# Optimization experiments

Measured on AMD Instinct MI355X. Metric: run time of the kernel, lower is better.

## Reference

```python
import jax, jax.numpy as jnp
import numpy as np

B, N, K = 1024, 200, 32
HID = 36
IN_DIM = K * (K + 2)  # k + q + flattened outer product


def setup_inputs() -> dict:
    key = jax.random.key(0)
    ks = jax.random.split(key, 4)
    candidate_ad = jax.random.normal(ks[0], (B, K), dtype=jnp.float32)
    goods = jax.random.normal(ks[1], (B, N, K), dtype=jnp.float32)
    W1 = jax.random.normal(ks[2], (IN_DIM, HID), dtype=jnp.float32) * (1.0 / np.sqrt(IN_DIM))
    b1 = jnp.zeros((HID,), dtype=jnp.float32)
    W2 = jax.random.normal(ks[3], (HID, 1), dtype=jnp.float32) * (1.0 / np.sqrt(HID))
    b2 = jnp.zeros((1,), dtype=jnp.float32)
    return {"candidate_ad": candidate_ad, "goods": goods, "W1": W1, "b1": b1, "W2": W2, "b2": b2}


def reference(candidate_ad, goods, W1, b1, W2, b2):
    # candidate_ad: [B, K] (attention key k), goods: [B, N, K] (queries q per item)
    Bs, Ns, Ks = goods.shape
    # outer product per item: einsum('bi,bj->bij', k, q) vectorized over N -> [B, N, K, K]
    outer = jnp.einsum('bi,bnj->bnij', candidate_ad, goods).reshape(Bs, Ns, Ks * Ks)
    k_b = jnp.broadcast_to(candidate_ad[:, None, :], (Bs, Ns, Ks))
    h1 = jnp.concatenate((k_b, goods, outer), axis=-1)          # [B, N, K*(K+2)]
    act = jax.nn.sigmoid(h1 @ W1 + b1)                           # [B, N, HID]
    weight = act @ W2 + b2                                       # [B, N, 1]
    out = jnp.sum(goods * weight, axis=1)                        # [B, K]
    return out
```

## Files before the change

### kernel.cpp

```cpp
#include <hip/hip_runtime.h>


#define BB 1024
#define BPB 4
#define NN 200
#define KK 32
#define HID 36
#define QP 40
#define LOG2E 1.44269504f

#define QBYTES (BPB * NN * KK * 4)
#define VOFF   QBYTES
#define COFF   (VOFF + 15360)
#define WOFF   (COFF + 768)
#define ROFF   (WOFF + 192)
#define SMEM_TOTAL (ROFF + 2048)

typedef __attribute__((ext_vector_type(8))) short bf16x8;
typedef __attribute__((ext_vector_type(4))) float f32x4;

__device__ __forceinline__ float rfl(float x) {
    return __uint_as_float(__builtin_amdgcn_readfirstlane(__float_as_uint(x)));
}
__device__ __forceinline__ unsigned short f2bf(float x) {
    unsigned int u = __float_as_uint(x);
    u = (u + 0x7fffu + ((u >> 16) & 1u)) >> 16;
    return (unsigned short)u;
}
__device__ __forceinline__ unsigned int pk_bf16(float lo, float hi) {
    unsigned int r;
    asm("v_cvt_pk_bf16_f32 %0, %1, %2" : "=v"(r) : "v"(lo), "v"(hi));
    return r;
}
__device__ __forceinline__ float fast_rcp(float x) {
#if __has_builtin(__builtin_amdgcn_rcpf)
    return __builtin_amdgcn_rcpf(x);
#else
    return 1.0f / x;
#endif
}
__device__ __forceinline__ float fast_exp2(float x) {
#if __has_builtin(__builtin_amdgcn_exp2f)
    return __builtin_amdgcn_exp2f(x);
#else
    return exp2f(x);
#endif
}

__global__ __launch_bounds__(1024, 4) void din_kernel(
    const float* __restrict__ cad,
    const float* __restrict__ goods,
    const float* __restrict__ W1,
    const float* __restrict__ b1p,
    const float* __restrict__ W2,
    const float* __restrict__ b2p,
    float* __restrict__ out)
{
    extern __shared__ char smem[];
    char*           Qlds = smem;
    unsigned short* V16  = (unsigned short*)(smem + VOFF);
    float*          c48  = (float*)(smem + COFF);
    float*          w248 = (float*)(smem + WOFF);
    float*          red_s = (float*)(smem + ROFF);

    const int tid  = threadIdx.x;
    const int b0   = blockIdx.x * BPB;
    const int lane = tid & 63;
    const int wv   = tid >> 6;
    const int l15  = lane & 15, lk = lane >> 4;
    const int bsel = wv & 3;
    const int mrow = wv >> 2;

    if (wv >= 6) {
        const char* gsrc = (const char*)(goods + (size_t)b0 * NN * KK);
        const int loff = (lane * 16) ^ ((lane >> 3) << 4);
        const int ubase = (wv - 6) * 10;
        #pragma unroll
        for (int j = 0; j < 10; ++j) {
            const int u = ubase + j;
            __builtin_amdgcn_global_load_lds(
                (const __attribute__((address_space(1))) void*)(gsrc + u * 1024 + loff),
                (__attribute__((address_space(3))) void*)(Qlds + u * 1024),
                16, 0, 0);
        }
    }

    const float* k0p = cad + b0 * KK;
    const float* k1p = k0p + KK;
    const float* k2p = k1p + KK;
    const float* k3p = k2p + KK;
    const float b2v = rfl(b2p[0]);

    const float4* W1q = reinterpret_cast<const float4*>(W1);
    if (tid < 288) {
        float4 acc0 = W1q[288 + tid];
        float4 acc1 = acc0, acc2 = acc0, acc3 = acc0;
        #pragma unroll 4
        for (int i = 0; i < KK; ++i) {
            const float4 w0 = W1q[576 + 288 * i + tid];
            const float ki0 = k0p[i], ki1 = k1p[i], ki2 = k2p[i], ki3 = k3p[i];
            acc0.x += ki0 * w0.x; acc0.y += ki0 * w0.y;
            acc0.z += ki0 * w0.z; acc0.w += ki0 * w0.w;
            acc1.x += ki1 * w0.x; acc1.y += ki1 * w0.y;
            acc1.z += ki1 * w0.z; acc1.w += ki1 * w0.w;
            acc2.x += ki2 * w0.x; acc2.y += ki2 * w0.y;
            acc2.z += ki2 * w0.z; acc2.w += ki2 * w0.w;
            acc3.x += ki3 * w0.x; acc3.y += ki3 * w0.y;
            acc3.z += ki3 * w0.z; acc3.w += ki3 * w0.w;
        }
        const float a0[4] = {acc0.x, acc0.y, acc0.z, acc0.w};
        const float a1[4] = {acc1.x, acc1.y, acc1.z, acc1.w};
        const float a2[4] = {acc2.x, acc2.y, acc2.z, acc2.w};
        const float a3[4] = {acc3.x, acc3.y, acc3.z, acc3.w};
        #pragma unroll
        for (int q = 0; q < 4; ++q) {
            const int e = 4 * tid + q, j = e / 36, h = e - 36 * j;
            const int o = h * QP + j;
            V16[0 * 1920 + o] = f2bf(a0[q]);
            V16[1 * 1920 + o] = f2bf(a1[q]);
            V16[2 * 1920 + o] = f2bf(a2[q]);
            V16[3 * 1920 + o] = f2bf(a3[q]);
        }
    } else if (tid < 324) {
        const int u = tid - 288, bl = u / 9, hq = u % 9;
        const float* kp = cad + (b0 + bl) * KK;
        float4 acc = reinterpret_cast<const float4*>(b1p)[hq];
        #pragma unroll 4
        for (int i = 0; i < KK; ++i) {
            const float ki = kp[i];
            const float4 wc = W1q[i * 9 + hq];
            acc.x += ki * wc.x; acc.y += ki * wc.y;
            acc.z += ki * wc.z; acc.w += ki * wc.w;
        }
        float4 cp4;
        cp4.x = -acc.x * LOG2E; cp4.y = -acc.y * LOG2E;
        cp4.z = -acc.z * LOG2E; cp4.w = -acc.w * LOG2E;
        *reinterpret_cast<float4*>(&c48[bl * 48 + 4 * hq]) = cp4;
    } else if (tid < 336) {
        const int u = tid - 324, bl = u / 3, q = u % 3;
        *reinterpret_cast<float4*>(&c48[bl * 48 + 36 + 4 * q]) =
            make_float4(0.f, 0.f, 0.f, 0.f);
    } else if (tid < 348) {
        const int u = tid - 336;
        if (u < 9)
            *reinterpret_cast<float4*>(&w248[4 * u]) =
                reinterpret_cast<const float4*>(W2)[u];
        else
            *reinterpret_cast<float4*>(&w248[36 + 4 * (u - 9)]) =
                make_float4(0.f, 0.f, 0.f, 0.f);
    } else if (tid < 732) {
        const int p = tid - 348;
        const int word = p % 192, pair = p / 192;
        const int w = (36 + (word >> 4)) * (QP / 2) + (word & 15);
        ((unsigned int*)V16)[(2 * pair + 0) * 960 + w] = 0u;
        ((unsigned int*)V16)[(2 * pair + 1) * 960 + w] = 0u;
    }
    __syncthreads();

    bf16x8 bfr[3];
    #pragma unroll
    for (int nt = 0; nt < 3; ++nt)
        bfr[nt] = *reinterpret_cast<const bf16x8*>(
            V16 + bsel * 1920 + (nt * 16 + l15) * QP + lk * 8);
    const float* cb = c48 + bsel * 48;

    float facc[8] = {0.f, 0.f, 0.f, 0.f, 0.f, 0.f, 0.f, 0.f};

    auto tile = [&](const float4& qa, const float4& qb, int m, bool masked) {
        union { unsigned int u[4]; bf16x8 v; } aq;
        aq.u[0] = pk_bf16(qa.x, qa.y);
        aq.u[1] = pk_bf16(qa.z, qa.w);
        aq.u[2] = pk_bf16(qb.x, qb.y);
        aq.u[3] = pk_bf16(qb.z, qb.w);
        const f32x4 zero = {0.f, 0.f, 0.f, 0.f};
        const f32x4 d0 = __builtin_amdgcn_mfma_f32_16x16x32_bf16(bfr[0], aq.v, zero, 0, 0, 0);
        const f32x4 d1 = __builtin_amdgcn_mfma_f32_16x16x32_bf16(bfr[1], aq.v, zero, 0, 0, 0);
        const f32x4 d2 = __builtin_amdgcn_mfma_f32_16x16x32_bf16(bfr[2], aq.v, zero, 0, 0, 0);

        const f32x4 c0 = *reinterpret_cast<const f32x4*>(cb + lk * 4);
        const f32x4 w0 = *reinterpret_cast<const f32x4*>(&w248[lk * 4]);
        const f32x4 c1 = *reinterpret_cast<const f32x4*>(cb + 16 + lk * 4);
        const f32x4 w1 = *reinterpret_cast<const f32x4*>(&w248[16 + lk * 4]);
        const f32x4 c2 = *reinterpret_cast<const f32x4*>(cb + 32 + lk * 4);
        const f32x4 w2 = *reinterpret_cast<const f32x4*>(&w248[32 + lk * 4]);

        float p = 0.f;
        #pragma unroll
        for (int r = 0; r < 4; ++r) {
            p += fast_rcp(1.0f + fast_exp2(__builtin_fmaf(d0[r], -LOG2E, c0[r]))) * w0[r];
            p += fast_rcp(1.0f + fast_exp2(__builtin_fmaf(d1[r], -LOG2E, c1[r]))) * w1[r];
            p += fast_rcp(1.0f + fast_exp2(__builtin_fmaf(d2[r], -LOG2E, c2[r]))) * w2[r];
        }
        p += __shfl_xor(p, 16, 64);
        p += __shfl_xor(p, 32, 64);

        float wn = b2v + p;
        if (masked) {
            const int n = m * 16 + l15;
            wn = (n < NN) ? wn : 0.f;
        }
        facc[0] += qa.x * wn; facc[1] += qa.y * wn;
        facc[2] += qa.z * wn; facc[3] += qa.w * wn;
        facc[4] += qb.x * wn; facc[5] += qb.y * wn;
        facc[6] += qb.z * wn; facc[7] += qb.w * wn;
    };

    #pragma unroll
    for (int t = 0; t < 4; ++t) {
        const int m = mrow + 4 * t;
        if (m < 13) {
            int row = m * 16 + l15;
            row = (row < NN) ? row : (NN - 1);
            const int rlin  = bsel * NN + row;
            const int byte0 = rlin * 128 + lk * 32;
            const int swz   = (rlin & 7) << 4;
            const float4 qa = *reinterpret_cast<const float4*>(Qlds + (byte0 ^ swz));
            const float4 qb = *reinterpret_cast<const float4*>(Qlds + ((byte0 + 16) ^ swz));
            tile(qa, qb, m, m == 12);
        }
    }

    #pragma unroll
    for (int s = 1; s <= 8; s <<= 1) {
        #pragma unroll
        for (int u = 0; u < 8; ++u)
            facc[u] += __shfl_xor(facc[u], s, 64);
    }
    if (l15 == 0) {
        #pragma unroll
        for (int u = 0; u < 8; ++u)
            red_s[(bsel * 4 + mrow) * KK + lk * 8 + u] = facc[u];
    }
    __syncthreads();

    if (tid < BPB * KK) {
        const int bl = tid >> 5, j = tid & 31;
        float s = 0.f;
        #pragma unroll
        for (int g = 0; g < 4; ++g) s += red_s[(bl * 4 + g) * KK + j];
        out[(b0 + bl) * KK + j] = s;
    }
}

extern "C" void kernel_launch(void* const* d_in, const int* in_sizes, int n_in,
                              void* d_out, int out_size, void* d_ws, size_t ws_size,
                              hipStream_t stream) {
    const float* cad   = (const float*)d_in[0];
    const float* goods = (const float*)d_in[1];
    const float* W1    = (const float*)d_in[2];
    const float* b1    = (const float*)d_in[3];
    const float* W2    = (const float*)d_in[4];
    const float* b2    = (const float*)d_in[5];
    float* outp = (float*)d_out;

    static bool attr_set = false;
    if (!attr_set) {
        (void)hipFuncSetAttribute((const void*)din_kernel,
                                  hipFuncAttributeMaxDynamicSharedMemorySize,
                                  SMEM_TOTAL);
        attr_set = true;
    }

    din_kernel<<<BB / BPB, 1024, SMEM_TOTAL, stream>>>(cad, goods, W1, b1, W2, b2, outp);
}
```

Before: 15.30 us.

## Split goods LDS prefetch into two phases and overlap second with compute

Reorders the asynchronous global-to-LDS loads of the goods tile so the first 128 rows per batch element arrive before the first barrier. That barrier now waits only with vmcnt(4) instead of a full drain. The first two row tiles are computed while the remaining loads are still in flight, and a second barrier after vmcnt(0) guards the rest. Load work is also redistributed across the loader waves. The aim is to hide part of the global load latency behind the MFMA and sigmoid work. The cost is an extra barrier and reliance on hand-written waitcnt assembly being correct.

Measured after the change: 16.34 us. +6.8%, slower.

```diff
diff --git a/kernel.cpp b/kernel.cpp
--- a/kernel.cpp
+++ b/kernel.cpp
@@ -71,17 +71,34 @@
     const int bsel = wv & 3;
     const int mrow = wv >> 2;
 
+    const float b2v = rfl(b2p[0]);
+    asm volatile("" :: "s"(b2v));
+
     if (wv >= 6) {
         const char* gsrc = (const char*)(goods + (size_t)b0 * NN * KK);
         const int loff = (lane * 16) ^ ((lane >> 3) << 4);
-        const int ubase = (wv - 6) * 10;
-        #pragma unroll
-        for (int j = 0; j < 10; ++j) {
-            const int u = ubase + j;
-            __builtin_amdgcn_global_load_lds(
-                (const __attribute__((address_space(1))) void*)(gsrc + u * 1024 + loff),
-                (__attribute__((address_space(3))) void*)(Qlds + u * 1024),
-                16, 0, 0);
+        const int si = wv - 6;
+        if (si < 8) {
+            #pragma unroll
+            for (int j = 0; j < 8; ++j) {
+                const int g = si * 8 + j;
+                const int u = (g >> 4) * 25 + (g & 15);
+                __builtin_amdgcn_global_load_lds(
+                    (const __attribute__((address_space(1))) void*)(gsrc + u * 1024 + loff),
+                    (__attribute__((address_space(3))) void*)(Qlds + u * 1024),
+                    16, 0, 0);
+            }
+        }
+        if (si < 9) {
+            #pragma unroll
+            for (int j = 0; j < 4; ++j) {
+                const int g = si * 4 + j;
+                const int u = (g / 9) * 25 + 16 + (g % 9);
+                __builtin_amdgcn_global_load_lds(
+                    (const __attribute__((address_space(1))) void*)(gsrc + u * 1024 + loff),
+                    (__attribute__((address_space(3))) void*)(Qlds + u * 1024),
+                    16, 0, 0);
+            }
         }
     }
 
@@ -89,7 +106,6 @@
     const float* k1p = k0p + KK;
     const float* k2p = k1p + KK;
     const float* k3p = k2p + KK;
-    const float b2v = rfl(b2p[0]);
 
     const float4* W1q = reinterpret_cast<const float4*>(W1);
     if (tid < 288) {
@@ -155,7 +171,12 @@
         ((unsigned int*)V16)[(2 * pair + 0) * 960 + w] = 0u;
         ((unsigned int*)V16)[(2 * pair + 1) * 960 + w] = 0u;
     }
-    __syncthreads();
+
+    asm volatile("" ::: "memory");
+    asm volatile("s_waitcnt vmcnt(4) lgkmcnt(0)" ::: "memory");
+    __builtin_amdgcn_sched_barrier(0);
+    __builtin_amdgcn_s_barrier();
+    __builtin_amdgcn_sched_barrier(0);
 
     bf16x8 bfr[3];
     #pragma unroll
@@ -205,17 +226,36 @@
         facc[6] += qb.z * wn; facc[7] += qb.w * wn;
     };
 
+    auto ldq = [&](int m, float4& qa, float4& qb) {
+        int row = m * 16 + l15;
+        row = (row < NN) ? row : (NN - 1);
+        const int rlin  = bsel * NN + row;
+        const int byte0 = rlin * 128 + lk * 32;
+        const int swz   = (rlin & 7) << 4;
+        qa = *reinterpret_cast<const float4*>(Qlds + (byte0 ^ swz));
+        qb = *reinterpret_cast<const float4*>(Qlds + ((byte0 + 16) ^ swz));
+    };
+
     #pragma unroll
-    for (int t = 0; t < 4; ++t) {
+    for (int t = 0; t < 2; ++t) {
+        const int m = mrow + 4 * t;
+        float4 qa, qb;
+        ldq(m, qa, qb);
+        tile(qa, qb, m, false);
+    }
+
+    asm volatile("" ::: "memory");
+    asm volatile("s_waitcnt vmcnt(0)" ::: "memory");
+    __builtin_amdgcn_sched_barrier(0);
+    __builtin_amdgcn_s_barrier();
+    __builtin_amdgcn_sched_barrier(0);
+
+    #pragma unroll
+    for (int t = 2; t < 4; ++t) {
         const int m = mrow + 4 * t;
         if (m < 13) {
-            int row = m * 16 + l15;
-            row = (row < NN) ? row : (NN - 1);
-            const int rlin  = bsel * NN + row;
-            const int byte0 = rlin * 128 + lk * 32;
-            const int swz   = (rlin & 7) << 4;
-            const float4 qa = *reinterpret_cast<const float4*>(Qlds + (byte0 ^ swz));
-            const float4 qb = *reinterpret_cast<const float4*>(Qlds + ((byte0 + 16) ^ swz));
+            float4 qa, qb;
+            ldq(m, qa, qb);
             tile(qa, qb, m, m == 12);
         }
     }
```
